# Optimization experiments

Measured on AMD Instinct MI355X. Metric: run time of the kernel, lower is better.

The kernel has to match this reference:

```python
import jax, jax.numpy as jnp
import numpy as np

B, IN, H = 16384, 512, 512


def setup_inputs() -> dict:
    key = jax.random.key(0)
    ks = jax.random.split(key, 7)
    s_in = 1.0 / np.sqrt(IN)
    s_h = 1.0 / np.sqrt(H)
    return {
        "x": jax.random.normal(ks[0], (B, IN), jnp.float32),
        "h": jax.random.normal(ks[1], (B, H), jnp.float32),
        "c": jax.random.normal(ks[2], (B, H), jnp.float32),
        # packed gate weights, order [i, f, g, o] along last dim (4*H)
        "Wx": jax.random.normal(ks[3], (IN, 4 * H), jnp.float32) * s_in,
        "Wh": jax.random.normal(ks[4], (H, 4 * H), jnp.float32) * s_h,
        "bx": jax.random.normal(ks[5], (4 * H,), jnp.float32) * s_in,
        "bh": jax.random.normal(ks[6], (4 * H,), jnp.float32) * s_h,
    }


def reference(x, h, c, Wx, Wh, bx, bh):
    # one fused GEMM per input stream instead of 8 small linears; same math
    gates = x @ Wx + bx + h @ Wh + bh          # [B, 4H]
    gi, gf, gg, go = jnp.split(gates, 4, axis=-1)
    i = jax.nn.sigmoid(gi)
    f = jax.nn.sigmoid(gf)
    g = jnp.tanh(gg)
    o = jax.nn.sigmoid(go)
    c_new = f * c + i * g
    h_new = o * jnp.tanh(c_new)
    return (h_new, c_new)
```

## Files before the change

kernel.cpp:

```cpp
#include <hip/hip_runtime.h>
#include <hip/hip_bf16.h>

#define B_DIM   16384
#define IN_DIM  512
#define H_DIM   512
#define K_DIM   1024
#define N4H     2048
#define BH      (B_DIM * H_DIM)

typedef __attribute__((ext_vector_type(8))) short  short8;
typedef __attribute__((ext_vector_type(4))) short  short4v;
typedef __attribute__((ext_vector_type(4))) float  f32x4;

__device__ inline void async_load16(const void* g, void* l) {
    __builtin_amdgcn_global_load_lds(
        (const __attribute__((address_space(1))) void*)g,
        (__attribute__((address_space(3)))       void*)l, 16, 0, 0);
}

__device__ inline short bf16bits(float f) {
    __hip_bfloat16 b = __float2bfloat16(f);
    return *reinterpret_cast<short*>(&b);
}

__device__ inline float sigmoidf_(float v) {
    return 1.0f / (1.0f + __expf(-v));
}
__device__ inline float tanhf_(float v) {
    v = fminf(fmaxf(v, -30.f), 30.f);
    float e = __expf(2.f * v);
    return (e - 1.f) / (e + 1.f);
}

__global__ __launch_bounds__(256) void prep_all(
    const float* __restrict__ Wx, const float* __restrict__ Wh,
    const float* __restrict__ bx, const float* __restrict__ bh,
    const float* __restrict__ x,  const float* __restrict__ h,
    __hip_bfloat16* __restrict__ Wt, __hip_bfloat16* __restrict__ Axh,
    float* __restrict__ bias_p) {
    const int bid = blockIdx.x;
    const int t   = threadIdx.x;

    if (bid < 2048) {
        __shared__ __hip_bfloat16 tile[32][33];
        const int bk = bid & 31;
        const int bn = bid >> 5;
        const int kb = bk * 32, nb = bn * 32;
#pragma unroll
        for (int r = 0; r < 4; ++r) {
            int k_loc = r * 8 + (t >> 5);
            int n_loc = t & 31;
            int kg = kb + k_loc;
            float v = (kg < IN_DIM) ? Wx[(size_t)kg * N4H + nb + n_loc]
                                    : Wh[(size_t)(kg - IN_DIM) * N4H + nb + n_loc];
            tile[k_loc][n_loc] = __float2bfloat16(v);
        }
        __syncthreads();
        {
            int n_loc = t >> 3;
            int k_loc = (t & 7) * 4;
            int ng = nb + n_loc;
            int g  = ng >> 9;
            int c  = ng & 511;
            int row_out = (c >> 5) * 128 + g * 32 + (c & 31);
            short4v v4;
            v4.x = *reinterpret_cast<short*>(&tile[k_loc + 0][n_loc]);
            v4.y = *reinterpret_cast<short*>(&tile[k_loc + 1][n_loc]);
            v4.z = *reinterpret_cast<short*>(&tile[k_loc + 2][n_loc]);
            v4.w = *reinterpret_cast<short*>(&tile[k_loc + 3][n_loc]);
            *(short4v*)&Wt[(size_t)row_out * K_DIM + kb + k_loc] = v4;
        }
        if (bid < 8) {
            int ng = bid * 256 + t;
            int g  = ng >> 9;
            int c  = ng & 511;
            int ro = (c >> 5) * 128 + g * 32 + (c & 31);
            bias_p[ro] = bx[ng] + bh[ng];
        }
    } else {
        const int ab = bid - 2048;
        const int kq = t;
        const float* src = (kq < 128) ? (x + kq * 4)
                                      : (h + (size_t)(kq - 128) * 4);
#pragma unroll
        for (int j = 0; j < 8; ++j) {
            int m = ab * 8 + j;
            float4 v = *(const float4*)(src + (size_t)m * 512);
            short4v sv;
            sv.x = bf16bits(v.x);
            sv.y = bf16bits(v.y);
            sv.z = bf16bits(v.z);
            sv.w = bf16bits(v.w);
            *(short4v*)&Axh[(size_t)m * K_DIM + kq * 4] = sv;
        }
    }
}

__global__ __launch_bounds__(512, 2) void lstm_gemm8t(
    const float* __restrict__ c_in,
    const __hip_bfloat16* __restrict__ Axh,
    const __hip_bfloat16* __restrict__ Wt,
    const float* __restrict__ bias_p,
    float* __restrict__ out) {
    __shared__ __align__(16) __hip_bfloat16 lds_a[3][16384];
    __shared__ __align__(16) __hip_bfloat16 lds_b[3][8192];

    const int tid   = threadIdx.x;
    const int w     = tid >> 6;
    const int lane  = tid & 63;
    const int col16 = lane & 15;
    const int quad  = lane >> 4;
    const int wm    = w >> 1;
    const int wnn   = w & 1;

    const int jb    = blockIdx.x;
    const int xcd   = jb & 7;
    const int local = jb >> 3;
    const int bm    = xcd * 8 + (local >> 4);
    const int bn    = local & 15;

    f32x4 acc[4][4];
#pragma unroll
    for (int mi = 0; mi < 4; ++mi)
#pragma unroll
        for (int ni = 0; ni < 4; ++ni)
            acc[mi][ni] = (f32x4){0.f, 0.f, 0.f, 0.f};

    const __hip_bfloat16* Ab = Axh + (size_t)bm * 256 * K_DIM;
    const __hip_bfloat16* Bb = Wt  + (size_t)bn * 128 * K_DIM;

    const int rsub = lane >> 3;
    const int lg   = (lane & 7) ^ rsub;

    auto STAGE = [&](int buf, int kt) {
        char* ba = (char*)lds_a[buf] + w * 1024;
        char* bb = (char*)lds_b[buf] + w * 1024;
        const __hip_bfloat16* As = Ab + (size_t)(w * 8 + rsub) * K_DIM + kt * 64 + lg * 8;
        const __hip_bfloat16* Bs = Bb + (size_t)(w * 8 + rsub) * K_DIM + kt * 64 + lg * 8;
        async_load16(As,                      ba);
        async_load16(As +  64 * K_DIM,        ba + 8192);
        async_load16(As + 128 * K_DIM,        ba + 16384);
        async_load16(As + 192 * K_DIM,        ba + 24576);
        async_load16(Bs,                      bb);
        async_load16(Bs +  64 * K_DIM,        bb + 8192);
    };

    int arow[4], brow[4], kx[2];
#pragma unroll
    for (int mi = 0; mi < 4; ++mi)
        arow[mi] = (wm * 64 + mi * 16 + col16) * 128;
#pragma unroll
    for (int ni = 0; ni < 4; ++ni)
        brow[ni] = (ni * 32 + wnn * 16 + col16) * 128;
#pragma unroll
    for (int ks = 0; ks < 2; ++ks)
        kx[ks] = (ks * 64 + quad * 16) ^ ((col16 & 7) << 4);

    STAGE(0, 0);
    STAGE(1, 1);

    int cur = 0;
    for (int t = 0; t < 16; ++t) {
        if (t < 15) asm volatile("s_waitcnt vmcnt(6)" ::: "memory");
        else        asm volatile("s_waitcnt vmcnt(0)" ::: "memory");
        __builtin_amdgcn_s_barrier();
        __builtin_amdgcn_sched_barrier(0);

        if (t < 14) {
            const int nxt = (cur >= 1) ? cur - 1 : 2;
            STAGE(nxt, t + 2);
        }

        const char* la = (const char*)lds_a[cur];
        const char* lb = (const char*)lds_b[cur];

#pragma unroll
        for (int ks = 0; ks < 2; ++ks) {
            short8 afr[4], bfr[4];
#pragma unroll
            for (int mi = 0; mi < 4; ++mi)
                afr[mi] = *(const short8*)(la + arow[mi] + kx[ks]);
#pragma unroll
            for (int ni = 0; ni < 4; ++ni)
                bfr[ni] = *(const short8*)(lb + brow[ni] + kx[ks]);

            __builtin_amdgcn_s_setprio(1);
#pragma unroll
            for (int mi = 0; mi < 4; ++mi)
#pragma unroll
                for (int ni = 0; ni < 4; ++ni)
                    acc[mi][ni] = __builtin_amdgcn_mfma_f32_16x16x32_bf16(
                        afr[mi], bfr[ni], acc[mi][ni], 0, 0, 0);
            __builtin_amdgcn_s_setprio(0);
        }

        cur = (cur == 2) ? 0 : cur + 1;
    }

    float bias_v[4];
#pragma unroll
    for (int g = 0; g < 4; ++g)
        bias_v[g] = bias_p[bn * 128 + g * 32 + wnn * 16 + col16];

    const int hc_g = bn * 32 + wnn * 16 + col16;

#pragma unroll
    for (int mi = 0; mi < 4; ++mi) {
#pragma unroll
        for (int reg = 0; reg < 4; ++reg) {
            const int m_g = bm * 256 + wm * 64 + mi * 16 + quad * 4 + reg;
            float gi = acc[mi][0][reg] + bias_v[0];
            float gf = acc[mi][1][reg] + bias_v[1];
            float gg = acc[mi][2][reg] + bias_v[2];
            float go = acc[mi][3][reg] + bias_v[3];
            float iv = sigmoidf_(gi);
            float fv = sigmoidf_(gf);
            float gv = tanhf_(gg);
            float ov = sigmoidf_(go);
            float co = c_in[(size_t)m_g * H_DIM + hc_g];
            float cn = fv * co + iv * gv;
            float hn = ov * tanhf_(cn);
            out[(size_t)m_g * H_DIM + hc_g]      = hn;
            out[BH + (size_t)m_g * H_DIM + hc_g] = cn;
        }
    }
}

__global__ __launch_bounds__(256) void prep_weights_fb(
    const float* __restrict__ Wx, const float* __restrict__ Wh,
    const float* __restrict__ bx, const float* __restrict__ bh,
    __hip_bfloat16* __restrict__ Wt, float* __restrict__ bias_p) {
    __shared__ __hip_bfloat16 tile[32][33];
    const int bid = blockIdx.x;
    const int bk  = bid & 31;
    const int bn  = bid >> 5;
    const int t   = threadIdx.x;
    const int kb  = bk * 32, nb = bn * 32;
#pragma unroll
    for (int r = 0; r < 4; ++r) {
        int k_loc = r * 8 + (t >> 5);
        int n_loc = t & 31;
        int kg = kb + k_loc;
        float v = (kg < IN_DIM) ? Wx[(size_t)kg * N4H + nb + n_loc]
                                : Wh[(size_t)(kg - IN_DIM) * N4H + nb + n_loc];
        tile[k_loc][n_loc] = __float2bfloat16(v);
    }
    __syncthreads();
    {
        int n_loc = t >> 3;
        int k_loc = (t & 7) * 4;
        int ng = nb + n_loc;
        int g  = ng >> 9;
        int c  = ng & 511;
        int row_out = (c >> 5) * 128 + g * 32 + (c & 31);
        short4v v4;
        v4.x = *reinterpret_cast<short*>(&tile[k_loc + 0][n_loc]);
        v4.y = *reinterpret_cast<short*>(&tile[k_loc + 1][n_loc]);
        v4.z = *reinterpret_cast<short*>(&tile[k_loc + 2][n_loc]);
        v4.w = *reinterpret_cast<short*>(&tile[k_loc + 3][n_loc]);
        *(short4v*)&Wt[(size_t)row_out * K_DIM + kb + k_loc] = v4;
    }
    if (bid < 8) {
        int ng = bid * 256 + t;
        int g  = ng >> 9;
        int c  = ng & 511;
        int ro = (c >> 5) * 128 + g * 32 + (c & 31);
        bias_p[ro] = bx[ng] + bh[ng];
    }
}

__global__ __launch_bounds__(256, 3) void lstm_gemm_fb(
    const float* __restrict__ x, const float* __restrict__ h,
    const float* __restrict__ c_in,
    const __hip_bfloat16* __restrict__ Wt, const float* __restrict__ bias_p,
    float* __restrict__ out) {
    __shared__ __hip_bfloat16 lds_a[128 * 32];
    __shared__ __hip_bfloat16 lds_b[128 * 32];
    const int tid   = threadIdx.x;
    const int bn    = blockIdx.x & 15;
    const int bm    = blockIdx.x >> 4;
    const int w     = tid >> 6;
    const int lane  = tid & 63;
    const int col16 = lane & 15;
    const int quad  = lane >> 4;
    f32x4 acc[2][8];
#pragma unroll
    for (int mi = 0; mi < 2; ++mi)
#pragma unroll
        for (int ni = 0; ni < 8; ++ni)
            acc[mi][ni] = (f32x4){0.f, 0.f, 0.f, 0.f};
    const __hip_bfloat16* wt_base = Wt + (size_t)(bn * 128) * K_DIM;
    const int chunk0 = w * 2;
    const int e0     = chunk0 * 512 + lane * 8;
    const int bn_loc0 = e0 >> 5, bk_off0 = e0 & 31;
    const int e1     = (chunk0 + 1) * 512 + lane * 8;
    const int bn_loc1 = e1 >> 5, bk_off1 = e1 & 31;
    for (int kt = 0; kt < 32; ++kt) {
        const int kb = kt * 32;
        const float* aptr;
        int koff;
        if (kb < IN_DIM) { aptr = x; koff = kb; }
        else             { aptr = h; koff = kb - IN_DIM; }
        async_load16(wt_base + (size_t)bn_loc0 * K_DIM + kb + bk_off0,
                     (void*)(lds_b + chunk0 * 512));
        async_load16(wt_base + (size_t)bn_loc1 * K_DIM + kb + bk_off1,
                     (void*)(lds_b + (chunk0 + 1) * 512));
        float4 av[4];
#pragma unroll
        for (int j = 0; j < 4; ++j) {
            int cch = j * 256 + tid;
            int row = cch >> 3;
            int kq  = (cch & 7) * 4;
            av[j] = *(const float4*)(aptr + (size_t)(bm * 128 + row) * IN_DIM
                                     + koff + kq);
        }
#pragma unroll
        for (int j = 0; j < 4; ++j) {
            int cch = j * 256 + tid;
            int row = cch >> 3;
            int kq  = (cch & 7) * 4;
            short4v sv;
            sv.x = bf16bits(av[j].x);
            sv.y = bf16bits(av[j].y);
            sv.z = bf16bits(av[j].z);
            sv.w = bf16bits(av[j].w);
            *(short4v*)&lds_a[row * 32 + kq] = sv;
        }
        __syncthreads();
        short8 afr[2], bfr[8];
#pragma unroll
        for (int mi = 0; mi < 2; ++mi)
            afr[mi] = *(const short8*)&lds_a[(w * 32 + mi * 16 + col16) * 32 + quad * 8];
#pragma unroll
        for (int ni = 0; ni < 8; ++ni)
            bfr[ni] = *(const short8*)&lds_b[(ni * 16 + col16) * 32 + quad * 8];
#pragma unroll
        for (int mi = 0; mi < 2; ++mi)
#pragma unroll
            for (int ni = 0; ni < 8; ++ni)
                acc[mi][ni] = __builtin_amdgcn_mfma_f32_16x16x32_bf16(
                    afr[mi], bfr[ni], acc[mi][ni], 0, 0, 0);
        __syncthreads();
    }
    float bias_v[4][2];
#pragma unroll
    for (int g = 0; g < 4; ++g)
#pragma unroll
        for (int h2 = 0; h2 < 2; ++h2)
            bias_v[g][h2] = bias_p[bn * 128 + g * 32 + h2 * 16 + col16];
#pragma unroll
    for (int mi = 0; mi < 2; ++mi) {
#pragma unroll
        for (int reg = 0; reg < 4; ++reg) {
            const int m_g = bm * 128 + w * 32 + mi * 16 + quad * 4 + reg;
#pragma unroll
            for (int h2 = 0; h2 < 2; ++h2) {
                const int hc_g = bn * 32 + h2 * 16 + col16;
                float gi = acc[mi][0 + h2][reg] + bias_v[0][h2];
                float gf = acc[mi][2 + h2][reg] + bias_v[1][h2];
                float gg = acc[mi][4 + h2][reg] + bias_v[2][h2];
                float go = acc[mi][6 + h2][reg] + bias_v[3][h2];
                float iv = sigmoidf_(gi);
                float fv = sigmoidf_(gf);
                float gv = tanhf_(gg);
                float ov = sigmoidf_(go);
                float co = c_in[(size_t)m_g * H_DIM + hc_g];
                float cn = fv * co + iv * gv;
                float hn = ov * tanhf_(cn);
                out[(size_t)m_g * H_DIM + hc_g]      = hn;
                out[BH + (size_t)m_g * H_DIM + hc_g] = cn;
            }
        }
    }
}

extern "C" void kernel_launch(void* const* d_in, const int* in_sizes, int n_in,
                              void* d_out, int out_size, void* d_ws, size_t ws_size,
                              hipStream_t stream) {
    const float* x  = (const float*)d_in[0];
    const float* h  = (const float*)d_in[1];
    const float* c  = (const float*)d_in[2];
    const float* Wx = (const float*)d_in[3];
    const float* Wh = (const float*)d_in[4];
    const float* bx = (const float*)d_in[5];
    const float* bh = (const float*)d_in[6];

    const size_t wtBytes  = (size_t)N4H * K_DIM * 2;
    const size_t axhBytes = (size_t)B_DIM * K_DIM * 2;
    const size_t need     = wtBytes + axhBytes + (size_t)N4H * 4;

    if (ws_size >= need) {
        __hip_bfloat16* Wt  = (__hip_bfloat16*)d_ws;
        __hip_bfloat16* Axh = (__hip_bfloat16*)((char*)d_ws + wtBytes);
        float* bias_p = (float*)((char*)d_ws + wtBytes + axhBytes);
        prep_all<<<4096, 256, 0, stream>>>(Wx, Wh, bx, bh, x, h, Wt, Axh, bias_p);
        lstm_gemm8t<<<1024, 512, 0, stream>>>(c, Axh, Wt, bias_p, (float*)d_out);
    } else {
        __hip_bfloat16* Wt = (__hip_bfloat16*)d_ws;
        float* bias_p = (float*)((char*)d_ws + wtBytes);
        prep_weights_fb<<<2048, 256, 0, stream>>>(Wx, Wh, bx, bh, Wt, bias_p);
        lstm_gemm_fb<<<2048, 256, 0, stream>>>(x, h, c, Wt, bias_p, (float*)d_out);
    }
}
```

Measured before the change: 261.3 us.

## Enlarge GEMM tile to 256x256 with double-buffered four-phase LDS pipeline

Replaces the 256x128 block tile with a 256x256 tile, so each wave computes 128x64 outputs with 8x4 accumulators and the launch grid halves to 512 blocks. The triple-buffered 64-wide K staging becomes a double buffer split into two 32-wide K halves, with loads for the next tile interleaved across four barrier-separated MFMA phases and a new rotating LDS swizzle. This raises arithmetic intensity and cuts global and LDS traffic per FLOP, at the cost of higher register pressure, more barriers, and only 512 blocks, which may leave some CUs with uneven work.

```diff
diff --git a/kernel.cpp b/kernel.cpp
--- a/kernel.cpp
+++ b/kernel.cpp
@@ -96,119 +96,166 @@
     }
 }
 
-__global__ __launch_bounds__(512, 2) void lstm_gemm8t(
+__global__ __launch_bounds__(512, 2) void lstm_gemm256(
     const float* __restrict__ c_in,
     const __hip_bfloat16* __restrict__ Axh,
     const __hip_bfloat16* __restrict__ Wt,
     const float* __restrict__ bias_p,
     float* __restrict__ out) {
-    __shared__ __align__(16) __hip_bfloat16 lds_a[3][16384];
-    __shared__ __align__(16) __hip_bfloat16 lds_b[3][8192];
+    __shared__ __align__(16) __hip_bfloat16 lds_a[2][16384];
+    __shared__ __align__(16) __hip_bfloat16 lds_b[2][16384];
 
     const int tid   = threadIdx.x;
     const int w     = tid >> 6;
     const int lane  = tid & 63;
     const int col16 = lane & 15;
     const int quad  = lane >> 4;
-    const int wm    = w >> 1;
-    const int wnn   = w & 1;
+    const int wm    = w >> 2;
+    const int wn    = w & 3;
 
     const int jb    = blockIdx.x;
     const int xcd   = jb & 7;
     const int local = jb >> 3;
-    const int bm    = xcd * 8 + (local >> 4);
-    const int bn    = local & 15;
-
-    f32x4 acc[4][4];
-#pragma unroll
-    for (int mi = 0; mi < 4; ++mi)
+    const int bm    = xcd * 8 + (local >> 3);
+    const int bn    = local & 7;
+
+    f32x4 acc[8][4];
+#pragma unroll
+    for (int mi = 0; mi < 8; ++mi)
 #pragma unroll
         for (int ni = 0; ni < 4; ++ni)
             acc[mi][ni] = (f32x4){0.f, 0.f, 0.f, 0.f};
 
     const __hip_bfloat16* Ab = Axh + (size_t)bm * 256 * K_DIM;
-    const __hip_bfloat16* Bb = Wt  + (size_t)bn * 128 * K_DIM;
-
-    const int rsub = lane >> 3;
-    const int lg   = (lane & 7) ^ rsub;
-
-    auto STAGE = [&](int buf, int kt) {
-        char* ba = (char*)lds_a[buf] + w * 1024;
-        char* bb = (char*)lds_b[buf] + w * 1024;
-        const __hip_bfloat16* As = Ab + (size_t)(w * 8 + rsub) * K_DIM + kt * 64 + lg * 8;
-        const __hip_bfloat16* Bs = Bb + (size_t)(w * 8 + rsub) * K_DIM + kt * 64 + lg * 8;
-        async_load16(As,                      ba);
-        async_load16(As +  64 * K_DIM,        ba + 8192);
-        async_load16(As + 128 * K_DIM,        ba + 16384);
-        async_load16(As + 192 * K_DIM,        ba + 24576);
-        async_load16(Bs,                      bb);
-        async_load16(Bs +  64 * K_DIM,        bb + 8192);
-    };
-
-    int arow[4], brow[4], kx[2];
-#pragma unroll
-    for (int mi = 0; mi < 4; ++mi)
-        arow[mi] = (wm * 64 + mi * 16 + col16) * 128;
-#pragma unroll
-    for (int ni = 0; ni < 4; ++ni)
-        brow[ni] = (ni * 32 + wnn * 16 + col16) * 128;
-#pragma unroll
-    for (int ks = 0; ks < 2; ++ks)
-        kx[ks] = (ks * 64 + quad * 16) ^ ((col16 & 7) << 4);
-
-    STAGE(0, 0);
-    STAGE(1, 1);
-
-    int cur = 0;
+    const __hip_bfloat16* Bb = Wt  + (size_t)bn * 256 * K_DIM;
+
+    const int lq = ((tid & 3) - ((tid >> 3) & 3)) & 3;
+
+#define STAGE(LDSBUF, GBASE, KH, KT)  do {                                     \
+    const __hip_bfloat16* _s = (GBASE) + (size_t)(tid >> 2) * K_DIM            \
+                               + (KT) * 64 + (KH) * 32 + lq * 8;               \
+    char* _d = (char*)(LDSBUF) + (KH) * 16384 + w * 1024;                      \
+    async_load16(_s,                       _d);                                \
+    async_load16(_s + (size_t)128 * K_DIM, _d + 8192);                         \
+  } while (0)
+
+    int aoff[8], boff[4];
+#pragma unroll
+    for (int mi = 0; mi < 8; ++mi) {
+        int r = wm * 128 + mi * 16 + col16;
+        aoff[mi] = r * 64 + ((quad + ((r >> 1) & 3)) & 3) * 16;
+    }
+#pragma unroll
+    for (int ni = 0; ni < 4; ++ni) {
+        int r = (wn >> 1) * 128 + ni * 32 + (wn & 1) * 16 + col16;
+        boff[ni] = r * 64 + ((quad + ((r >> 1) & 3)) & 3) * 16;
+    }
+
+    STAGE(lds_a[0], Ab, 0, 0);
+    STAGE(lds_b[0], Bb, 0, 0);
+    STAGE(lds_a[0], Ab, 1, 0);
+    STAGE(lds_b[0], Bb, 1, 0);
+
+    short8 afrA[4], afrB[4], bfr[4];
+
+#define PHASE_MID()                                                            \
+    __builtin_amdgcn_sched_barrier(0);                                         \
+    __builtin_amdgcn_s_barrier();                                              \
+    asm volatile("s_waitcnt lgkmcnt(0)" ::: "memory");                         \
+    __builtin_amdgcn_sched_barrier(0);
+
     for (int t = 0; t < 16; ++t) {
-        if (t < 15) asm volatile("s_waitcnt vmcnt(6)" ::: "memory");
-        else        asm volatile("s_waitcnt vmcnt(0)" ::: "memory");
-        __builtin_amdgcn_s_barrier();
-        __builtin_amdgcn_sched_barrier(0);
-
-        if (t < 14) {
-            const int nxt = (cur >= 1) ? cur - 1 : 2;
-            STAGE(nxt, t + 2);
-        }
-
+        const int cur = t & 1;
         const char* la = (const char*)lds_a[cur];
         const char* lb = (const char*)lds_b[cur];
-
-#pragma unroll
-        for (int ks = 0; ks < 2; ++ks) {
-            short8 afr[4], bfr[4];
-#pragma unroll
-            for (int mi = 0; mi < 4; ++mi)
-                afr[mi] = *(const short8*)(la + arow[mi] + kx[ks]);
-#pragma unroll
-            for (int ni = 0; ni < 4; ++ni)
-                bfr[ni] = *(const short8*)(lb + brow[ni] + kx[ks]);
-
-            __builtin_amdgcn_s_setprio(1);
-#pragma unroll
-            for (int mi = 0; mi < 4; ++mi)
-#pragma unroll
-                for (int ni = 0; ni < 4; ++ni)
-                    acc[mi][ni] = __builtin_amdgcn_mfma_f32_16x16x32_bf16(
-                        afr[mi], bfr[ni], acc[mi][ni], 0, 0, 0);
-            __builtin_amdgcn_s_setprio(0);
-        }
-
-        cur = (cur == 2) ? 0 : cur + 1;
-    }
+        __hip_bfloat16* nxa = lds_a[cur ^ 1];
+        __hip_bfloat16* nxb = lds_b[cur ^ 1];
+        const bool pre = (t < 15);
+
+        asm volatile("s_waitcnt vmcnt(4)" ::: "memory");
+        __builtin_amdgcn_s_barrier();
+
+#pragma unroll
+        for (int q = 0; q < 4; ++q) afrA[q] = *(const short8*)(la + aoff[q]);
+#pragma unroll
+        for (int n = 0; n < 4; ++n) bfr[n] = *(const short8*)(lb + boff[n]);
+        if (pre) STAGE(nxa, Ab, 0, t + 1);
+        PHASE_MID();
+        __builtin_amdgcn_s_setprio(1);
+#pragma unroll
+        for (int q = 0; q < 4; ++q)
+#pragma unroll
+            for (int n = 0; n < 4; ++n)
+                acc[q][n] = __builtin_amdgcn_mfma_f32_16x16x32_bf16(
+                    afrA[q], bfr[n], acc[q][n], 0, 0, 0);
+        __builtin_amdgcn_s_setprio(0);
+        __builtin_amdgcn_sched_barrier(0);
+        __builtin_amdgcn_s_barrier();
+
+#pragma unroll
+        for (int q = 0; q < 4; ++q) afrB[q] = *(const short8*)(la + aoff[q + 4]);
+        if (pre) STAGE(nxb, Bb, 0, t + 1);
+        PHASE_MID();
+        __builtin_amdgcn_s_setprio(1);
+#pragma unroll
+        for (int q = 0; q < 4; ++q)
+#pragma unroll
+            for (int n = 0; n < 4; ++n)
+                acc[q + 4][n] = __builtin_amdgcn_mfma_f32_16x16x32_bf16(
+                    afrB[q], bfr[n], acc[q + 4][n], 0, 0, 0);
+        __builtin_amdgcn_s_setprio(0);
+        __builtin_amdgcn_sched_barrier(0);
+        if (pre) asm volatile("s_waitcnt vmcnt(4)" ::: "memory");
+        else     asm volatile("s_waitcnt vmcnt(0)" ::: "memory");
+        __builtin_amdgcn_s_barrier();
+
+#pragma unroll
+        for (int q = 0; q < 4; ++q) afrA[q] = *(const short8*)(la + 16384 + aoff[q]);
+#pragma unroll
+        for (int n = 0; n < 4; ++n) bfr[n] = *(const short8*)(lb + 16384 + boff[n]);
+        if (pre) STAGE(nxa, Ab, 1, t + 1);
+        PHASE_MID();
+        __builtin_amdgcn_s_setprio(1);
+#pragma unroll
+        for (int q = 0; q < 4; ++q)
+#pragma unroll
+            for (int n = 0; n < 4; ++n)
+                acc[q][n] = __builtin_amdgcn_mfma_f32_16x16x32_bf16(
+                    afrA[q], bfr[n], acc[q][n], 0, 0, 0);
+        __builtin_amdgcn_s_setprio(0);
+        __builtin_amdgcn_sched_barrier(0);
+        __builtin_amdgcn_s_barrier();
+
+#pragma unroll
+        for (int q = 0; q < 4; ++q) afrB[q] = *(const short8*)(la + 16384 + aoff[q + 4]);
+        if (pre) STAGE(nxb, Bb, 1, t + 1);
+        PHASE_MID();
+        __builtin_amdgcn_s_setprio(1);
+#pragma unroll
+        for (int q = 0; q < 4; ++q)
+#pragma unroll
+            for (int n = 0; n < 4; ++n)
+                acc[q + 4][n] = __builtin_amdgcn_mfma_f32_16x16x32_bf16(
+                    afrB[q], bfr[n], acc[q + 4][n], 0, 0, 0);
+        __builtin_amdgcn_s_setprio(0);
+        __builtin_amdgcn_sched_barrier(0);
+        __builtin_amdgcn_s_barrier();
+    }
+#undef STAGE
+#undef PHASE_MID
 
     float bias_v[4];
 #pragma unroll
     for (int g = 0; g < 4; ++g)
-        bias_v[g] = bias_p[bn * 128 + g * 32 + wnn * 16 + col16];
-
-    const int hc_g = bn * 32 + wnn * 16 + col16;
-
-#pragma unroll
-    for (int mi = 0; mi < 4; ++mi) {
+        bias_v[g] = bias_p[bn * 256 + (wn >> 1) * 128 + g * 32 + (wn & 1) * 16 + col16];
+
+    const int hc_g = bn * 64 + (wn >> 1) * 32 + (wn & 1) * 16 + col16;
+
+#pragma unroll
+    for (int mi = 0; mi < 8; ++mi) {
 #pragma unroll
         for (int reg = 0; reg < 4; ++reg) {
-            const int m_g = bm * 256 + wm * 64 + mi * 16 + quad * 4 + reg;
+            const int m_g = bm * 256 + wm * 128 + mi * 16 + quad * 4 + reg;
             float gi = acc[mi][0][reg] + bias_v[0];
             float gf = acc[mi][1][reg] + bias_v[1];
             float gg = acc[mi][2][reg] + bias_v[2];
@@ -394,7 +441,7 @@
         __hip_bfloat16* Axh = (__hip_bfloat16*)((char*)d_ws + wtBytes);
         float* bias_p = (float*)((char*)d_ws + wtBytes + axhBytes);
         prep_all<<<4096, 256, 0, stream>>>(Wx, Wh, bx, bh, x, h, Wt, Axh, bias_p);
-        lstm_gemm8t<<<1024, 512, 0, stream>>>(c, Axh, Wt, bias_p, (float*)d_out);
+        lstm_gemm256<<<512, 512, 0, stream>>>(c, Axh, Wt, bias_p, (float*)d_out);
     } else {
         __hip_bfloat16* Wt = (__hip_bfloat16*)d_ws;
         float* bias_p = (float*)((char*)d_ws + wtBytes);
```

After: 243.0 us. 7.0% less time.
